# Kernel optimization log

Hardware: AMD Instinct MI355X
Metric: run time of the kernel (lower is better)

Reference implementation:

```python
import jax
import jax.numpy as jnp
from jax import lax
import numpy as np

BATCH, SEQ, STATES = 64, 4096, 64


def setup_inputs() -> dict:
    key = jax.random.key(0)
    k1, k2, k3, k4 = jax.random.split(key, 4)
    scores = jax.random.normal(k1, (BATCH, SEQ, STATES), dtype=jnp.float32)
    transition = jax.random.normal(k2, (STATES, STATES), dtype=jnp.float32)
    source = jax.random.uniform(k3, (STATES,), dtype=jnp.float32)
    sink = jax.random.uniform(k4, (STATES,), dtype=jnp.float32)
    return {"scores": scores, "transition": transition, "source": source, "sink": sink}


def reference(scores, transition, source, sink):
    # Linear-chain CRF log-partition (forward algorithm in log space).
    # scores: (B, T, S) emission scores; transition: (S, S) [from, to].
    B, T, S = scores.shape
    # t == 0: original code logsumexps a broadcast-identical axis of size S,
    # which adds a constant log(S) -- reproduced here for bit-faithful math.
    score0 = source[None, :] + scores[:, 0] + jnp.log(jnp.asarray(S, scores.dtype))  # (B, S)

    def step(alpha, s_t):
        # alpha: (B, S) log-scores over previous state; s_t: (B, S) emissions at t
        new = jax.nn.logsumexp(alpha[:, :, None] + transition[None, :, :], axis=1) + s_t
        return new, None

    # scan over time: (T-1, B, S)
    alpha_final, _ = lax.scan(step, score0, jnp.swapaxes(scores[:, 1:], 0, 1))
    return jax.nn.logsumexp(alpha_final + sink[None, :], axis=1)  # (B,)
```

## Files before the change

### kernel.cpp

```cpp
#include <hip/hip_runtime.h>
#include <cstdint>


#define B_    64
#define T_    4096
#define S_    64
#define L_    35
#define NC_   117
#define CPB_  128
#define WPB_  8
#define NTILE_ (B_ * WPB_ * L_)
#define LOG2E 1.44269504088896340736f

typedef float  f32x4  __attribute__((ext_vector_type(4)));
typedef __bf16 bf16x8 __attribute__((ext_vector_type(8)));

union U4B { uint4 u; bf16x8 b; };

__device__ __forceinline__ unsigned rne_bf16(float f) {
    unsigned x = __float_as_uint(f);
    return (x + 0x7FFFu + ((x >> 16) & 1u)) >> 16;
}

__global__ __launch_bounds__(256) void crf_prep(
    const float* __restrict__ scores, unsigned short* __restrict__ P4)
{
    __shared__ float tile[4][16][65];
    const int wl   = threadIdx.x >> 6;
    const int lane = threadIdx.x & 63;
    const int wid  = blockIdx.x * 4 + wl;
    const int b  = wid / (WPB_ * L_);
    const int r0 = wid % (WPB_ * L_);
    const int g8 = r0 / L_;
    const int tt = r0 % L_;

    #pragma unroll
    for (int m = 0; m < 16; ++m) {
        int c = g8 * 16 + m;
        float v = 0.0f;
        if (c < NC_) v = scores[((size_t)b * T_ + (1 + L_ * c + tt)) * S_ + lane];
        tile[wl][m][lane] = v;
    }
    __builtin_amdgcn_s_waitcnt(0xC07F);
    __builtin_amdgcn_wave_barrier();

    const int g = lane >> 4, l = lane & 15;
    unsigned out[8];
    #pragma unroll
    for (int d = 0; d < 8; ++d) {
        int j0 = 2 * d, j1 = 2 * d + 1;
        float f0 = exp2f(tile[wl][4 * g + (j0 & 3)][16 * (j0 >> 2) + l] * LOG2E);
        float f1 = exp2f(tile[wl][4 * g + (j1 & 3)][16 * (j1 >> 2) + l] * LOG2E);
        out[d] = rne_bf16(f0) | (rne_bf16(f1) << 16);
    }
    uint4* dst = (uint4*)(P4 + (size_t)wid * 1024) + lane * 2;
    dst[0] = make_uint4(out[0], out[1], out[2], out[3]);
    dst[1] = make_uint4(out[4], out[5], out[6], out[7]);
}

__global__ __launch_bounds__(64, 2) void crf_phase1(
    const float* __restrict__ transition,
    const unsigned short* __restrict__ P4,
    float* __restrict__ Ybuf, float* __restrict__ Zbuf, float* __restrict__ Lz)
{
    __shared__ float tb[2][16][68];
    const int w   = blockIdx.x;
    const bool bwd = w >= (B_ * WPB_);
    const int wg  = bwd ? w - B_ * WPB_ : w;
    const int b   = wg >> 3;
    const int g8  = wg & 7;
    const int lane = threadIdx.x;
    const int g = lane >> 4, l = lane & 15;

    bf16x8 BE[2][4];
    #pragma unroll
    for (int kb = 0; kb < 2; ++kb)
    #pragma unroll
    for (int nt = 0; nt < 4; ++nt) {
        unsigned pk[4];
        #pragma unroll
        for (int dd = 0; dd < 4; ++dd) {
            int k0 = 32 * kb + 8 * g + 2 * dd;
            int n  = 16 * nt + l;
            float e0, e1;
            if (!bwd) { e0 = transition[k0 * 64 + n]; e1 = transition[(k0 + 1) * 64 + n]; }
            else      { e0 = transition[n * 64 + k0]; e1 = transition[n * 64 + k0 + 1]; }
            pk[dd] = rne_bf16(exp2f(e0 * LOG2E)) | (rne_bf16(exp2f(e1 * LOG2E)) << 16);
        }
        U4B t; t.u = make_uint4(pk[0], pk[1], pk[2], pk[3]);
        BE[kb][nt] = t.b;
    }

    const size_t tbase = (size_t)(b * WPB_ + g8) * L_;
    const uint4* tp = (const uint4*)P4;

    f32x4 acc[4];
    #pragma unroll
    for (int nt = 0; nt < 4; ++nt) acc[nt] = {1.f, 1.f, 1.f, 1.f};
    int Lt[4] = {0, 0, 0, 0};

    auto ldtile = [&](int tt, uint4& x, uint4& y) {
        const uint4* p = tp + (tbase + tt) * 128 + lane * 2;
        x = p[0]; y = p[1];
    };
    auto emmul = [&](const uint4& c0, const uint4& c1) {
        unsigned dw[8] = {c0.x, c0.y, c0.z, c0.w, c1.x, c1.y, c1.z, c1.w};
        #pragma unroll
        for (int nt = 0; nt < 4; ++nt)
            #pragma unroll
            for (int r = 0; r < 4; ++r) {
                unsigned d = dw[2 * nt + (r >> 1)];
                float em = (r & 1) ? __uint_as_float(d & 0xFFFF0000u)
                                   : __uint_as_float(d << 16);
                acc[nt][r] *= em;
            }
    };
    auto renorm = [&]() {
        #pragma unroll
        for (int r = 0; r < 4; ++r) {
            float m = fmaxf(fmaxf(acc[0][r], acc[1][r]), fmaxf(acc[2][r], acc[3][r]));
            m = fmaxf(m, __shfl_xor(m, 1, 64));
            m = fmaxf(m, __shfl_xor(m, 2, 64));
            m = fmaxf(m, __shfl_xor(m, 4, 64));
            m = fmaxf(m, __shfl_xor(m, 8, 64));
            int ex = (int)(__float_as_uint(m) >> 23) - 127;
            float sc = __uint_as_float((unsigned)(127 - ex) << 23);
            Lt[r] += ex;
            #pragma unroll
            for (int nt = 0; nt < 4; ++nt) acc[nt][r] *= sc;
        }
    };
    auto transpose_mfma = [&](int buf) {
        #pragma unroll
        for (int nt = 0; nt < 4; ++nt)
            #pragma unroll
            for (int r = 0; r < 4; ++r)
                tb[buf][4 * g + r][16 * nt + l] = acc[nt][r];
        __builtin_amdgcn_s_waitcnt(0xC07F);
        __builtin_amdgcn_wave_barrier();
        bf16x8 A[2];
        #pragma unroll
        for (int kb = 0; kb < 2; ++kb) {
            const float* rowp = &tb[buf][l][32 * kb + 8 * g];
            float4 x = *(const float4*)rowp;
            float4 y = *(const float4*)(rowp + 4);
            U4B t;
            t.u.x = (__float_as_uint(x.x) >> 16) | (__float_as_uint(x.y) & 0xFFFF0000u);
            t.u.y = (__float_as_uint(x.z) >> 16) | (__float_as_uint(x.w) & 0xFFFF0000u);
            t.u.z = (__float_as_uint(y.x) >> 16) | (__float_as_uint(y.y) & 0xFFFF0000u);
            t.u.w = (__float_as_uint(y.z) >> 16) | (__float_as_uint(y.w) & 0xFFFF0000u);
            A[kb] = t.b;
        }
        #pragma unroll
        for (int nt = 0; nt < 4; ++nt) {
            f32x4 z4 = {0.f, 0.f, 0.f, 0.f};
            z4      = __builtin_amdgcn_mfma_f32_16x16x32_bf16(A[0], BE[0][nt], z4, 0, 0, 0);
            acc[nt] = __builtin_amdgcn_mfma_f32_16x16x32_bf16(A[1], BE[1][nt], z4, 0, 0, 0);
        }
    };

    if (!bwd) {
        uint4 pa0, pb0, pa1, pb1;
        ldtile(0, pa0, pb0);
        ldtile(1, pa1, pb1);
        for (int tt = 0; tt < L_; ++tt) {
            uint4 c0 = pa0, c1 = pb0;
            pa0 = pa1; pb0 = pb1;
            int tn = tt + 2; if (tn > L_ - 1) tn = L_ - 1;
            ldtile(tn, pa1, pb1);
            transpose_mfma(tt & 1);
            emmul(c0, c1);
            if ((tt & 3) == 3) renorm();
        }
        float* yb = Ybuf + ((size_t)b * CPB_ + g8 * 16) * 64;
        #pragma unroll
        for (int nt = 0; nt < 4; ++nt)
            #pragma unroll
            for (int r = 0; r < 4; ++r)
                yb[(4 * g + r) * 64 + 16 * nt + l] = acc[nt][r];
    } else {
        uint4 pa0, pb0, pa1, pb1;
        ldtile(L_ - 1, pa0, pb0);
        ldtile(L_ - 2, pa1, pb1);
        for (int i = 0; i < L_; ++i) {
            uint4 c0 = pa0, c1 = pb0;
            pa0 = pa1; pb0 = pb1;
            int tn = L_ - 1 - i - 2; if (tn < 0) tn = 0;
            ldtile(tn, pa1, pb1);
            emmul(c0, c1);
            if ((i & 3) == 3) renorm();
            transpose_mfma(i & 1);
        }
        float* zb = Zbuf + ((size_t)b * CPB_ + g8 * 16) * 64;
        #pragma unroll
        for (int nt = 0; nt < 4; ++nt)
            #pragma unroll
            for (int r = 0; r < 4; ++r)
                zb[(4 * g + r) * 64 + 16 * nt + l] = acc[nt][r];
        if (l == 0) {
            #pragma unroll
            for (int r = 0; r < 4; ++r)
                Lz[b * CPB_ + g8 * 16 + 4 * g + r] = (float)Lt[r];
        }
    }
}

__global__ __launch_bounds__(256) void crf_phase2(
    const float* __restrict__ scores, const float* __restrict__ source,
    const float* __restrict__ sink,
    const float* __restrict__ Ybuf, const float* __restrict__ Zbuf,
    const float* __restrict__ Lz, float* __restrict__ out)
{
    __shared__ float part[4];
    const int b = blockIdx.x;
    const int wv = threadIdx.x >> 6;
    const int lane = threadIdx.x & 63;
    const float esink = exp2f(sink[lane] * LOG2E);

    float acc = 0.f;
    for (int c = wv; c < NC_; c += 4) {
        float yh = Ybuf[((size_t)b * CPB_ + c) * 64 + lane];
        float nx = (c < NC_ - 1) ? Zbuf[((size_t)b * CPB_ + c + 1) * 64 + lane] : esink;
        float p = yh * nx, q = yh;
        #pragma unroll
        for (int m = 32; m >= 1; m >>= 1) {
            p += __shfl_xor(p, m, 64);
            q += __shfl_xor(q, m, 64);
        }
        acc += log2f(p) - log2f(q) + Lz[b * CPB_ + c];
    }
    if (wv == 0) {
        float a0 = exp2f((source[lane] + scores[(size_t)b * T_ * S_ + lane]) * LOG2E);
        float p = a0 * Zbuf[((size_t)b * CPB_) * 64 + lane];
        #pragma unroll
        for (int m = 32; m >= 1; m >>= 1) p += __shfl_xor(p, m, 64);
        acc += log2f(p);
    }
    if (lane == 0) part[wv] = acc;
    __syncthreads();
    if (threadIdx.x == 0)
        out[b] = 0.6931471805599453f * (part[0] + part[1] + part[2] + part[3])
               + 4.158883083359672f;
}

extern "C" void kernel_launch(void* const* d_in, const int* in_sizes, int n_in,
                              void* d_out, int out_size, void* d_ws, size_t ws_size,
                              hipStream_t stream) {
    (void)in_sizes; (void)n_in; (void)out_size; (void)ws_size;
    const float* scores     = (const float*)d_in[0];
    const float* transition = (const float*)d_in[1];
    const float* source     = (const float*)d_in[2];
    const float* sink       = (const float*)d_in[3];
    float* out = (float*)d_out;

    unsigned short* P4 = (unsigned short*)d_ws;
    float* Ybuf = (float*)((char*)d_ws + (size_t)NTILE_ * 2048);
    float* Zbuf = Ybuf + (size_t)B_ * CPB_ * 64;
    float* Lz   = Zbuf + (size_t)B_ * CPB_ * 64;

    hipLaunchKernelGGL(crf_prep,   dim3(NTILE_ / 4), dim3(256), 0, stream, scores, P4);
    hipLaunchKernelGGL(crf_phase1, dim3(2 * B_ * WPB_), dim3(64), 0, stream,
                       transition, P4, Ybuf, Zbuf, Lz);
    hipLaunchKernelGGL(crf_phase2, dim3(B_), dim3(256), 0, stream,
                       scores, source, sink, Ybuf, Zbuf, Lz, out);
}
```

Baseline: 150.9 us.

## Fuse emission exp into phase1 and shorten chunks for more parallelism

New measurement: 138.0 us. 8.5% less time.

```diff
diff --git a/kernel.cpp b/kernel.cpp
--- a/kernel.cpp
+++ b/kernel.cpp
@@ -5,72 +5,35 @@
 #define B_    64
 #define T_    4096
 #define S_    64
-#define L_    35
-#define NC_   117
-#define CPB_  128
-#define WPB_  8
-#define NTILE_ (B_ * WPB_ * L_)
+#define L_    15
+#define NC_   273
+#define WPB_  18
+#define CPB_  288
 #define LOG2E 1.44269504088896340736f
 
 typedef float  f32x4  __attribute__((ext_vector_type(4)));
 typedef __bf16 bf16x8 __attribute__((ext_vector_type(8)));
-
 union U4B { uint4 u; bf16x8 b; };
 
 __device__ __forceinline__ unsigned rne_bf16(float f) {
     unsigned x = __float_as_uint(f);
     return (x + 0x7FFFu + ((x >> 16) & 1u)) >> 16;
 }
-
-__global__ __launch_bounds__(256) void crf_prep(
-    const float* __restrict__ scores, unsigned short* __restrict__ P4)
-{
-    __shared__ float tile[4][16][65];
-    const int wl   = threadIdx.x >> 6;
-    const int lane = threadIdx.x & 63;
-    const int wid  = blockIdx.x * 4 + wl;
-    const int b  = wid / (WPB_ * L_);
-    const int r0 = wid % (WPB_ * L_);
-    const int g8 = r0 / L_;
-    const int tt = r0 % L_;
-
-    #pragma unroll
-    for (int m = 0; m < 16; ++m) {
-        int c = g8 * 16 + m;
-        float v = 0.0f;
-        if (c < NC_) v = scores[((size_t)b * T_ + (1 + L_ * c + tt)) * S_ + lane];
-        tile[wl][m][lane] = v;
-    }
-    __builtin_amdgcn_s_waitcnt(0xC07F);
-    __builtin_amdgcn_wave_barrier();
-
-    const int g = lane >> 4, l = lane & 15;
-    unsigned out[8];
-    #pragma unroll
-    for (int d = 0; d < 8; ++d) {
-        int j0 = 2 * d, j1 = 2 * d + 1;
-        float f0 = exp2f(tile[wl][4 * g + (j0 & 3)][16 * (j0 >> 2) + l] * LOG2E);
-        float f1 = exp2f(tile[wl][4 * g + (j1 & 3)][16 * (j1 >> 2) + l] * LOG2E);
-        out[d] = rne_bf16(f0) | (rne_bf16(f1) << 16);
-    }
-    uint4* dst = (uint4*)(P4 + (size_t)wid * 1024) + lane * 2;
-    dst[0] = make_uint4(out[0], out[1], out[2], out[3]);
-    dst[1] = make_uint4(out[4], out[5], out[6], out[7]);
-}
-
-__global__ __launch_bounds__(64, 2) void crf_phase1(
+__device__ __forceinline__ unsigned pk2(float a, float b) {
+    return rne_bf16(a) | (rne_bf16(b) << 16);
+}
+
+__global__ __launch_bounds__(64, 3) void crf_phase1(
+    const float* __restrict__ scores,
     const float* __restrict__ transition,
-    const unsigned short* __restrict__ P4,
     float* __restrict__ Ybuf, float* __restrict__ Zbuf, float* __restrict__ Lz)
 {
     __shared__ float tb[2][16][68];
-    const int w   = blockIdx.x;
-    const bool bwd = w >= (B_ * WPB_);
-    const int wg  = bwd ? w - B_ * WPB_ : w;
-    const int b   = wg >> 3;
-    const int g8  = wg & 7;
-    const int lane = threadIdx.x;
-    const int g = lane >> 4, l = lane & 15;
+    const int wid  = blockIdx.x;
+    const bool bwd = wid >= (B_ * WPB_);
+    const int wl   = bwd ? wid - B_ * WPB_ : wid;
+    const int b    = wl / WPB_, wg = wl % WPB_;
+    const int lane = threadIdx.x, g = lane >> 4, l = lane & 15;
 
     bf16x8 BE[2][4];
     #pragma unroll
@@ -80,40 +43,28 @@
         unsigned pk[4];
         #pragma unroll
         for (int dd = 0; dd < 4; ++dd) {
-            int k0 = 32 * kb + 8 * g + 2 * dd;
-            int n  = 16 * nt + l;
+            int k0 = 32 * kb + 8 * g + 2 * dd, n = 16 * nt + l;
             float e0, e1;
             if (!bwd) { e0 = transition[k0 * 64 + n]; e1 = transition[(k0 + 1) * 64 + n]; }
             else      { e0 = transition[n * 64 + k0]; e1 = transition[n * 64 + k0 + 1]; }
-            pk[dd] = rne_bf16(exp2f(e0 * LOG2E)) | (rne_bf16(exp2f(e1 * LOG2E)) << 16);
-        }
-        U4B t; t.u = make_uint4(pk[0], pk[1], pk[2], pk[3]);
-        BE[kb][nt] = t.b;
-    }
-
-    const size_t tbase = (size_t)(b * WPB_ + g8) * L_;
-    const uint4* tp = (const uint4*)P4;
+            pk[dd] = pk2(exp2f(e0 * LOG2E), exp2f(e1 * LOG2E));
+        }
+        U4B t; t.u = make_uint4(pk[0], pk[1], pk[2], pk[3]); BE[kb][nt] = t.b;
+    }
+
+    int cl = 16 * wg + l; if (cl > NC_ - 1) cl = NC_ - 1;
+    const float* ap = scores + ((size_t)b * T_ + 15 * cl + (bwd ? 15 : 0)) * S_ + 8 * g;
 
     f32x4 acc[4];
-    #pragma unroll
-    for (int nt = 0; nt < 4; ++nt) acc[nt] = {1.f, 1.f, 1.f, 1.f};
     int Lt[4] = {0, 0, 0, 0};
 
-    auto ldtile = [&](int tt, uint4& x, uint4& y) {
-        const uint4* p = tp + (tbase + tt) * 128 + lane * 2;
-        x = p[0]; y = p[1];
-    };
-    auto emmul = [&](const uint4& c0, const uint4& c1) {
-        unsigned dw[8] = {c0.x, c0.y, c0.z, c0.w, c1.x, c1.y, c1.z, c1.w};
-        #pragma unroll
-        for (int nt = 0; nt < 4; ++nt)
-            #pragma unroll
-            for (int r = 0; r < 4; ++r) {
-                unsigned d = dw[2 * nt + (r >> 1)];
-                float em = (r & 1) ? __uint_as_float(d & 0xFFFF0000u)
-                                   : __uint_as_float(d << 16);
-                acc[nt][r] *= em;
-            }
+    auto mfma8 = [&](bf16x8 A0, bf16x8 A1) {
+        #pragma unroll
+        for (int nt = 0; nt < 4; ++nt) {
+            f32x4 z4 = {0.f, 0.f, 0.f, 0.f};
+            z4      = __builtin_amdgcn_mfma_f32_16x16x32_bf16(A0, BE[0][nt], z4, 0, 0, 0);
+            acc[nt] = __builtin_amdgcn_mfma_f32_16x16x32_bf16(A1, BE[1][nt], z4, 0, 0, 0);
+        }
     };
     auto renorm = [&]() {
         #pragma unroll
@@ -130,95 +81,110 @@
             for (int nt = 0; nt < 4; ++nt) acc[nt][r] *= sc;
         }
     };
-    auto transpose_mfma = [&](int buf) {
+    auto xposeA = [&](int par, const f32x4& c0, const f32x4& c1,
+                      const f32x4& c2, const f32x4& c3, bf16x8& A0, bf16x8& A1) {
+        float (*tp)[68] = tb[par];
         #pragma unroll
         for (int nt = 0; nt < 4; ++nt)
             #pragma unroll
             for (int r = 0; r < 4; ++r)
-                tb[buf][4 * g + r][16 * nt + l] = acc[nt][r];
+                tp[4 * g + r][16 * nt + l] = acc[nt][r];
         __builtin_amdgcn_s_waitcnt(0xC07F);
         __builtin_amdgcn_wave_barrier();
-        bf16x8 A[2];
-        #pragma unroll
-        for (int kb = 0; kb < 2; ++kb) {
-            const float* rowp = &tb[buf][l][32 * kb + 8 * g];
-            float4 x = *(const float4*)rowp;
-            float4 y = *(const float4*)(rowp + 4);
-            U4B t;
-            t.u.x = (__float_as_uint(x.x) >> 16) | (__float_as_uint(x.y) & 0xFFFF0000u);
-            t.u.y = (__float_as_uint(x.z) >> 16) | (__float_as_uint(x.w) & 0xFFFF0000u);
-            t.u.z = (__float_as_uint(y.x) >> 16) | (__float_as_uint(y.y) & 0xFFFF0000u);
-            t.u.w = (__float_as_uint(y.z) >> 16) | (__float_as_uint(y.w) & 0xFFFF0000u);
-            A[kb] = t.b;
-        }
-        #pragma unroll
-        for (int nt = 0; nt < 4; ++nt) {
-            f32x4 z4 = {0.f, 0.f, 0.f, 0.f};
-            z4      = __builtin_amdgcn_mfma_f32_16x16x32_bf16(A[0], BE[0][nt], z4, 0, 0, 0);
-            acc[nt] = __builtin_amdgcn_mfma_f32_16x16x32_bf16(A[1], BE[1][nt], z4, 0, 0, 0);
-        }
+        const float* rowp = &tp[l][8 * g];
+        f32x4 x0 = *(const f32x4*)rowp;
+        f32x4 x1 = *(const f32x4*)(rowp + 4);
+        f32x4 x2 = *(const f32x4*)(rowp + 32);
+        f32x4 x3 = *(const f32x4*)(rowp + 36);
+        U4B t0, t1;
+        t0.u.x = pk2(x0[0] * exp2f(c0[0] * LOG2E), x0[1] * exp2f(c0[1] * LOG2E));
+        t0.u.y = pk2(x0[2] * exp2f(c0[2] * LOG2E), x0[3] * exp2f(c0[3] * LOG2E));
+        t0.u.z = pk2(x1[0] * exp2f(c1[0] * LOG2E), x1[1] * exp2f(c1[1] * LOG2E));
+        t0.u.w = pk2(x1[2] * exp2f(c1[2] * LOG2E), x1[3] * exp2f(c1[3] * LOG2E));
+        t1.u.x = pk2(x2[0] * exp2f(c2[0] * LOG2E), x2[1] * exp2f(c2[1] * LOG2E));
+        t1.u.y = pk2(x2[2] * exp2f(c2[2] * LOG2E), x2[3] * exp2f(c2[3] * LOG2E));
+        t1.u.z = pk2(x3[0] * exp2f(c3[0] * LOG2E), x3[1] * exp2f(c3[1] * LOG2E));
+        t1.u.w = pk2(x3[2] * exp2f(c3[2] * LOG2E), x3[3] * exp2f(c3[3] * LOG2E));
+        A0 = t0.b; A1 = t1.b;
+    };
+    auto ldq = [&](int idx, f32x4& q0, f32x4& q1, f32x4& q2, f32x4& q3) {
+        const float* p = ap + (ptrdiff_t)idx * S_;
+        q0 = *(const f32x4*)p;        q1 = *(const f32x4*)(p + 4);
+        q2 = *(const f32x4*)(p + 32); q3 = *(const f32x4*)(p + 36);
     };
 
     if (!bwd) {
-        uint4 pa0, pb0, pa1, pb1;
-        ldtile(0, pa0, pb0);
-        ldtile(1, pa1, pb1);
-        for (int tt = 0; tt < L_; ++tt) {
-            uint4 c0 = pa0, c1 = pb0;
-            pa0 = pa1; pb0 = pb1;
-            int tn = tt + 2; if (tn > L_ - 1) tn = L_ - 1;
-            ldtile(tn, pa1, pb1);
-            transpose_mfma(tt & 1);
-            emmul(c0, c1);
+        f32x4 q0, q1, q2, q3;
+        ldq(1, q0, q1, q2, q3);
+        { U4B t; t.u = make_uint4(0x3F803F80u, 0x3F803F80u, 0x3F803F80u, 0x3F803F80u);
+          mfma8(t.b, t.b); }
+        #pragma unroll 2
+        for (int tt = 1; tt < L_; ++tt) {
+            f32x4 c0 = q0, c1 = q1, c2 = q2, c3 = q3;
+            if (tt + 1 < L_) ldq(tt + 1, q0, q1, q2, q3);
+            bf16x8 A0, A1;
+            xposeA(tt & 1, c0, c1, c2, c3, A0, A1);
+            mfma8(A0, A1);
             if ((tt & 3) == 3) renorm();
         }
-        float* yb = Ybuf + ((size_t)b * CPB_ + g8 * 16) * 64;
-        #pragma unroll
-        for (int nt = 0; nt < 4; ++nt)
-            #pragma unroll
-            for (int r = 0; r < 4; ++r)
-                yb[(4 * g + r) * 64 + 16 * nt + l] = acc[nt][r];
+        #pragma unroll
+        for (int r = 0; r < 4; ++r) {
+            int c = 16 * wg + 4 * g + r; int cc = c > NC_ - 1 ? NC_ - 1 : c;
+            const float* bp = scores + ((size_t)b * T_ + 15 * cc + 15) * S_ + l;
+            float* yb = Ybuf + ((size_t)b * CPB_ + c) * S_ + l;
+            #pragma unroll
+            for (int nt = 0; nt < 4; ++nt)
+                yb[16 * nt] = acc[nt][r] * exp2f(bp[16 * nt] * LOG2E);
+        }
     } else {
-        uint4 pa0, pb0, pa1, pb1;
-        ldtile(L_ - 1, pa0, pb0);
-        ldtile(L_ - 2, pa1, pb1);
-        for (int i = 0; i < L_; ++i) {
-            uint4 c0 = pa0, c1 = pb0;
-            pa0 = pa1; pb0 = pb1;
-            int tn = L_ - 1 - i - 2; if (tn < 0) tn = 0;
-            ldtile(tn, pa1, pb1);
-            emmul(c0, c1);
+        f32x4 q0, q1, q2, q3, n0, n1, n2, n3;
+        ldq(0, q0, q1, q2, q3);
+        ldq(-1, n0, n1, n2, n3);
+        {
+            U4B t0, t1;
+            t0.u.x = pk2(exp2f(q0[0] * LOG2E), exp2f(q0[1] * LOG2E));
+            t0.u.y = pk2(exp2f(q0[2] * LOG2E), exp2f(q0[3] * LOG2E));
+            t0.u.z = pk2(exp2f(q1[0] * LOG2E), exp2f(q1[1] * LOG2E));
+            t0.u.w = pk2(exp2f(q1[2] * LOG2E), exp2f(q1[3] * LOG2E));
+            t1.u.x = pk2(exp2f(q2[0] * LOG2E), exp2f(q2[1] * LOG2E));
+            t1.u.y = pk2(exp2f(q2[2] * LOG2E), exp2f(q2[3] * LOG2E));
+            t1.u.z = pk2(exp2f(q3[0] * LOG2E), exp2f(q3[1] * LOG2E));
+            t1.u.w = pk2(exp2f(q3[2] * LOG2E), exp2f(q3[3] * LOG2E));
+            mfma8(t0.b, t1.b);
+        }
+        #pragma unroll 2
+        for (int i = 1; i < L_; ++i) {
+            f32x4 c0 = n0, c1 = n1, c2 = n2, c3 = n3;
+            if (i + 1 < L_) ldq(-(i + 1), n0, n1, n2, n3);
+            bf16x8 A0, A1;
+            xposeA(i & 1, c0, c1, c2, c3, A0, A1);
+            mfma8(A0, A1);
             if ((i & 3) == 3) renorm();
-            transpose_mfma(i & 1);
-        }
-        float* zb = Zbuf + ((size_t)b * CPB_ + g8 * 16) * 64;
-        #pragma unroll
-        for (int nt = 0; nt < 4; ++nt)
-            #pragma unroll
-            for (int r = 0; r < 4; ++r)
-                zb[(4 * g + r) * 64 + 16 * nt + l] = acc[nt][r];
-        if (l == 0) {
-            #pragma unroll
-            for (int r = 0; r < 4; ++r)
-                Lz[b * CPB_ + g8 * 16 + 4 * g + r] = (float)Lt[r];
-        }
-    }
-}
-
-__global__ __launch_bounds__(256) void crf_phase2(
+        }
+        #pragma unroll
+        for (int r = 0; r < 4; ++r) {
+            int c = 16 * wg + 4 * g + r;
+            float* zb = Zbuf + ((size_t)b * CPB_ + c) * S_ + l;
+            #pragma unroll
+            for (int nt = 0; nt < 4; ++nt) zb[16 * nt] = acc[nt][r];
+            if (l == 0) Lz[b * CPB_ + c] = (float)Lt[r];
+        }
+    }
+}
+
+__global__ __launch_bounds__(512) void crf_phase2(
     const float* __restrict__ scores, const float* __restrict__ source,
     const float* __restrict__ sink,
     const float* __restrict__ Ybuf, const float* __restrict__ Zbuf,
     const float* __restrict__ Lz, float* __restrict__ out)
 {
-    __shared__ float part[4];
+    __shared__ float part[8];
     const int b = blockIdx.x;
-    const int wv = threadIdx.x >> 6;
-    const int lane = threadIdx.x & 63;
+    const int wv = threadIdx.x >> 6, lane = threadIdx.x & 63;
     const float esink = exp2f(sink[lane] * LOG2E);
 
     float acc = 0.f;
-    for (int c = wv; c < NC_; c += 4) {
+    for (int c = wv; c < NC_; c += 8) {
         float yh = Ybuf[((size_t)b * CPB_ + c) * 64 + lane];
         float nx = (c < NC_ - 1) ? Zbuf[((size_t)b * CPB_ + c + 1) * 64 + lane] : esink;
         float p = yh * nx, q = yh;
@@ -238,9 +204,12 @@
     }
     if (lane == 0) part[wv] = acc;
     __syncthreads();
-    if (threadIdx.x == 0)
-        out[b] = 0.6931471805599453f * (part[0] + part[1] + part[2] + part[3])
-               + 4.158883083359672f;
+    if (threadIdx.x == 0) {
+        float s = 0.f;
+        #pragma unroll
+        for (int i = 0; i < 8; ++i) s += part[i];
+        out[b] = 0.6931471805599453f * s + 4.158883083359672f;
+    }
 }
 
 extern "C" void kernel_launch(void* const* d_in, const int* in_sizes, int n_in,
@@ -253,14 +222,12 @@
     const float* sink       = (const float*)d_in[3];
     float* out = (float*)d_out;
 
-    unsigned short* P4 = (unsigned short*)d_ws;
-    float* Ybuf = (float*)((char*)d_ws + (size_t)NTILE_ * 2048);
+    float* Ybuf = (float*)d_ws;
     float* Zbuf = Ybuf + (size_t)B_ * CPB_ * 64;
     float* Lz   = Zbuf + (size_t)B_ * CPB_ * 64;
 
-    hipLaunchKernelGGL(crf_prep,   dim3(NTILE_ / 4), dim3(256), 0, stream, scores, P4);
     hipLaunchKernelGGL(crf_phase1, dim3(2 * B_ * WPB_), dim3(64), 0, stream,
-                       transition, P4, Ybuf, Zbuf, Lz);
-    hipLaunchKernelGGL(crf_phase2, dim3(B_), dim3(256), 0, stream,
+                       scores, transition, Ybuf, Zbuf, Lz);
+    hipLaunchKernelGGL(crf_phase2, dim3(B_), dim3(512), 0, stream,
                        scores, source, sink, Ybuf, Zbuf, Lz, out);
 }
```
